# Kernel tuning notes

Hardware: AMD Instinct MI355X
Metric: run time of the kernel (lower is better)

Reference implementation:

```python
import jax, jax.numpy as jnp
import numpy as np

SIZE = 5   # local window side
HEADS = 1

def patch_extract(x, size):
    # x: [B, C, H, W] -> [B, C, size*size, H, W], replicate padding,
    # window index l = i*size + j (row-major over kernel), matching F.unfold.
    p = size // 2
    xp = jnp.pad(x, ((0, 0), (0, 0), (p, p), (p, p)), mode='edge')
    H, W = x.shape[2], x.shape[3]
    windows = [xp[:, :, i:i + H, j:j + W] for i in range(size) for j in range(size)]
    return jnp.stack(windows, axis=2)

def setup_inputs() -> dict:
    key = jax.random.key(0)
    k1, k2, k3, k4 = jax.random.split(key, 4)
    B, C, H, W = 4, 128, 64, 128
    attn = jax.random.normal(k1, (B, HEADS, H * W, SIZE * SIZE), dtype=jnp.float32)
    fmap = jax.random.normal(k2, (B, C, H, W), dtype=jnp.float32)
    Wv = jax.random.normal(k3, (C, C), dtype=jnp.float32) * (1.0 / np.sqrt(C))
    gamma = jax.random.normal(k4, (1,), dtype=jnp.float32)
    return {"attn": attn, "fmap": fmap, "Wv": Wv, "gamma": gamma}

def reference(attn, fmap, Wv, gamma):
    B, C, H, W = fmap.shape
    d = C // HEADS
    L = SIZE * SIZE
    # to_v: 1x1 conv, no bias
    v = jnp.einsum('oc,bchw->bohw', Wv, fmap)
    # local window gather: [B, C, L, H, W]
    v = patch_extract(v, SIZE)
    # 'b (h d) l x y -> b h (x y) d l'
    v = v.reshape(B, HEADS, d, L, H, W)
    v = v.transpose(0, 1, 4, 5, 2, 3).reshape(B, HEADS, H * W, d, L)
    # weighted sum over the local window
    out = jnp.einsum('bhnl,bhndl->bhnd', attn, v)
    # 'b h (x y) d -> b (h d) x y'
    out = out.reshape(B, HEADS, H, W, d).transpose(0, 1, 4, 2, 3).reshape(B, C, H, W)
    return fmap + gamma[0] * out
```

## Files before the change

### kernel.cpp

```cpp
#include <hip/hip_runtime.h>


namespace {
constexpr int Bn = 4, Cn = 128, Hn = 64, Wn = 128, Ln = 25;
constexpr int HWn = Hn * Wn;

constexpr int TY = 4, TX = 16;
constexpr int HY = 8, HX = 24;
constexpr int RS = 136;
constexpr int SVS = 136;
constexpr int WVS = 136;
constexpr int NT = 512;

typedef __attribute__((ext_vector_type(8))) short short8;
typedef __attribute__((ext_vector_type(4))) float f32x4;

__device__ inline unsigned short f2bf(float f) {
    unsigned u = __float_as_uint(f);
    return (unsigned short)((u + 0x7fffu + ((u >> 16) & 1u)) >> 16);
}

__global__ __launch_bounds__(NT, 4) void lsa_fused(
    const float* __restrict__ attn, const float* __restrict__ fmap,
    const float* __restrict__ Wv, const float* __restrict__ gamma,
    float* __restrict__ out)
{
    __shared__ alignas(16) unsigned short hs[HY * HX * RS];
    __shared__ alignas(16) unsigned short sv[TY * TX * SVS];
    __shared__ float at_s[TY * TX * Ln];

    const int tid = threadIdx.x;
    const int b = blockIdx.z;
    const int x0 = blockIdx.x * TX;
    const int y0 = blockIdx.y * TY;

    for (int i = tid; i < HY * 64 * 6; i += NT) {
        const int k = i % 6;
        const int r = i / 6;
        const int cp = r & 63;
        const int dy = r >> 6;
        const int ry = min(max(y0 + dy - 2, 0), Hn - 1);
        const int gxb = x0 - 4 + 4 * k;
        const size_t rowb = ((size_t)(b * Cn + 2 * cp)) * HWn + (size_t)ry * Wn;
        float4 va, vb;
        if (gxb < 0) {
            const float s0 = fmap[rowb], s1 = fmap[rowb + HWn];
            va.x = va.y = va.z = va.w = s0;
            vb.x = vb.y = vb.z = vb.w = s1;
        } else if (gxb > Wn - 4) {
            const float s0 = fmap[rowb + Wn - 1], s1 = fmap[rowb + HWn + Wn - 1];
            va.x = va.y = va.z = va.w = s0;
            vb.x = vb.y = vb.z = vb.w = s1;
        } else {
            va = *(const float4*)&fmap[rowb + gxb];
            vb = *(const float4*)&fmap[rowb + HWn + gxb];
        }
        unsigned short* hbase = &hs[(dy * HX + 4 * k) * RS + 2 * cp];
        *(unsigned*)&hbase[0 * RS] = (unsigned)f2bf(va.x) | ((unsigned)f2bf(vb.x) << 16);
        *(unsigned*)&hbase[1 * RS] = (unsigned)f2bf(va.y) | ((unsigned)f2bf(vb.y) << 16);
        *(unsigned*)&hbase[2 * RS] = (unsigned)f2bf(va.z) | ((unsigned)f2bf(vb.z) << 16);
        *(unsigned*)&hbase[3 * RS] = (unsigned)f2bf(va.w) | ((unsigned)f2bf(vb.w) << 16);
    }
    {
        const size_t ab = ((size_t)b * HWn + (size_t)y0 * Wn + x0) * Ln;
        for (int i = tid; i < TY * TX * Ln; i += NT) {
            const int yi = i / 400, j = i - yi * 400;
            at_s[i] = attn[ab + (size_t)yi * (Wn * Ln) + j];
        }
    }
    __syncthreads();

    const int xi = tid & 15, kq = (tid >> 4) & 7, yi = tid >> 7;
    const int p = yi * 16 + xi;
    float acc[16];
#pragma unroll
    for (int j = 0; j < 16; ++j) acc[j] = 0.f;

#pragma unroll
    for (int l = 0; l < Ln; ++l) {
        const int dy = l / 5, dx = l % 5;
        const float a = at_s[p * Ln + l];
        const unsigned short* row = &hs[((yi + dy) * HX + (2 + xi + dx)) * RS + kq * 16];
#pragma unroll
        for (int q = 0; q < 2; ++q) {
            uint4 u = *(const uint4*)&row[q * 8];
            const unsigned w[4] = {u.x, u.y, u.z, u.w};
#pragma unroll
            for (int e = 0; e < 4; ++e) {
                acc[q * 8 + 2 * e + 0] += a * __uint_as_float(w[e] << 16);
                acc[q * 8 + 2 * e + 1] += a * __uint_as_float(w[e] & 0xffff0000u);
            }
        }
    }
    {
        unsigned short* dst = &sv[p * SVS + kq * 16];
#pragma unroll
        for (int q = 0; q < 2; ++q) {
            unsigned pk[4];
#pragma unroll
            for (int e = 0; e < 4; ++e)
                pk[e] = (unsigned)f2bf(acc[q * 8 + 2 * e]) |
                        ((unsigned)f2bf(acc[q * 8 + 2 * e + 1]) << 16);
            uint4 v; v.x = pk[0]; v.y = pk[1]; v.z = pk[2]; v.w = pk[3];
            *(uint4*)&dst[q * 8] = v;
        }
    }
    __syncthreads();

#pragma unroll
    for (int t = 0; t < 8; ++t) {
        const int i4 = tid + t * NT;
        const float4 w = *(const float4*)&Wv[(size_t)i4 * 4];
        const int r = i4 >> 5;
        const int c = (i4 & 31) * 4;
        uint2 v;
        v.x = (unsigned)f2bf(w.x) | ((unsigned)f2bf(w.y) << 16);
        v.y = (unsigned)f2bf(w.z) | ((unsigned)f2bf(w.w) << 16);
        *(uint2*)&hs[r * WVS + c] = v;
    }
    __syncthreads();

    const int wave = tid >> 6, lane = tid & 63;
    const int m16 = lane & 15, q = lane >> 4;
    const int wrow = wave >> 1;
    const int mhalf = wave & 1;
    const int n = (y0 + wrow) * Wn + x0 + m16;
    const float g = gamma[0];

    short8 bfrag[4];
    {
        const unsigned short* srow = &sv[(wrow * 16 + m16) * SVS + q * 8];
#pragma unroll
        for (int kk = 0; kk < 4; ++kk) bfrag[kk] = *(const short8*)(srow + kk * 32);
    }
    f32x4 accv[4];
#pragma unroll
    for (int t = 0; t < 4; ++t) { f32x4 z = {0.f, 0.f, 0.f, 0.f}; accv[t] = z; }

#pragma unroll
    for (int t = 0; t < 4; ++t) {
        const int mg = mhalf * 4 + t;
        const unsigned short* arow = &hs[(mg * 16 + m16) * WVS + q * 8];
#pragma unroll
        for (int kk = 0; kk < 4; ++kk) {
            short8 af = *(const short8*)(arow + kk * 32);
            accv[t] = __builtin_amdgcn_mfma_f32_16x16x32_bf16(af, bfrag[kk], accv[t], 0, 0, 0);
        }
    }

#pragma unroll
    for (int t = 0; t < 4; ++t) {
        const int mg = mhalf * 4 + t;
#pragma unroll
        for (int r = 0; r < 4; ++r) {
            const int c = mg * 16 + q * 4 + r;
            const size_t idx = ((size_t)(b * Cn + c)) * HWn + n;
            out[idx] = fmap[idx] + g * accv[t][r];
        }
    }
}
}

extern "C" void kernel_launch(void* const* d_in, const int* in_sizes, int n_in,
                              void* d_out, int out_size, void* d_ws, size_t ws_size,
                              hipStream_t stream) {
    const float* attn  = (const float*)d_in[0];
    const float* fmap  = (const float*)d_in[1];
    const float* Wv    = (const float*)d_in[2];
    const float* gamma = (const float*)d_in[3];
    float* out = (float*)d_out;

    dim3 grid(Wn / TX, Hn / TY, Bn);
    lsa_fused<<<grid, NT, 0, stream>>>(attn, fmap, Wv, gamma, out);
}
```

Measured before the change: 98.97 us.

## Batch global loads into registers before LDS stores and swizzle block order

The halo fill now issues all six fmap load pairs and the attn tile load into registers before any conversion or LDS write. The attn load becomes a single float4 per thread. The Wv load is hoisted above the sv pack so its latency overlaps that work. The 3D grid is flattened to 512 blocks and remapped so neighbouring block IDs spread across spatial tiles, intended to balance L2 or XCD locality. The extra live float4 registers raise register pressure under the 4-blocks-per-SIMD launch bound and may cause spills.

Measured after the change: 90.20 us. 8.9% less time.

```diff
diff --git a/kernel.cpp b/kernel.cpp
--- a/kernel.cpp
+++ b/kernel.cpp
@@ -27,14 +27,23 @@
 {
     __shared__ alignas(16) unsigned short hs[HY * HX * RS];
     __shared__ alignas(16) unsigned short sv[TY * TX * SVS];
-    __shared__ float at_s[TY * TX * Ln];
+    __shared__ alignas(16) float at_s[TY * TX * Ln];
 
     const int tid = threadIdx.x;
-    const int b = blockIdx.z;
-    const int x0 = blockIdx.x * TX;
-    const int y0 = blockIdx.y * TY;
 
-    for (int i = tid; i < HY * 64 * 6; i += NT) {
+    const unsigned bid = blockIdx.x;
+    const unsigned logical = (bid & 7u) * 64u + (bid >> 3);
+    const int bx  = logical & 7;
+    const int byz = logical >> 3;
+    const int by  = byz & 15;
+    const int b   = byz >> 4;
+    const int x0 = bx * TX;
+    const int y0 = by * TY;
+
+    float4 va[6], vb[6];
+#pragma unroll
+    for (int t = 0; t < 6; ++t) {
+        const int i = tid + t * NT;
         const int k = i % 6;
         const int r = i / 6;
         const int cp = r & 63;
@@ -42,32 +51,40 @@
         const int ry = min(max(y0 + dy - 2, 0), Hn - 1);
         const int gxb = x0 - 4 + 4 * k;
         const size_t rowb = ((size_t)(b * Cn + 2 * cp)) * HWn + (size_t)ry * Wn;
-        float4 va, vb;
         if (gxb < 0) {
             const float s0 = fmap[rowb], s1 = fmap[rowb + HWn];
-            va.x = va.y = va.z = va.w = s0;
-            vb.x = vb.y = vb.z = vb.w = s1;
+            va[t].x = va[t].y = va[t].z = va[t].w = s0;
+            vb[t].x = vb[t].y = vb[t].z = vb[t].w = s1;
         } else if (gxb > Wn - 4) {
             const float s0 = fmap[rowb + Wn - 1], s1 = fmap[rowb + HWn + Wn - 1];
-            va.x = va.y = va.z = va.w = s0;
-            vb.x = vb.y = vb.z = vb.w = s1;
+            va[t].x = va[t].y = va[t].z = va[t].w = s0;
+            vb[t].x = vb[t].y = vb[t].z = vb[t].w = s1;
         } else {
-            va = *(const float4*)&fmap[rowb + gxb];
-            vb = *(const float4*)&fmap[rowb + HWn + gxb];
-        }
-        unsigned short* hbase = &hs[(dy * HX + 4 * k) * RS + 2 * cp];
-        *(unsigned*)&hbase[0 * RS] = (unsigned)f2bf(va.x) | ((unsigned)f2bf(vb.x) << 16);
-        *(unsigned*)&hbase[1 * RS] = (unsigned)f2bf(va.y) | ((unsigned)f2bf(vb.y) << 16);
-        *(unsigned*)&hbase[2 * RS] = (unsigned)f2bf(va.z) | ((unsigned)f2bf(vb.z) << 16);
-        *(unsigned*)&hbase[3 * RS] = (unsigned)f2bf(va.w) | ((unsigned)f2bf(vb.w) << 16);
-    }
-    {
-        const size_t ab = ((size_t)b * HWn + (size_t)y0 * Wn + x0) * Ln;
-        for (int i = tid; i < TY * TX * Ln; i += NT) {
-            const int yi = i / 400, j = i - yi * 400;
-            at_s[i] = attn[ab + (size_t)yi * (Wn * Ln) + j];
+            va[t] = *(const float4*)&fmap[rowb + gxb];
+            vb[t] = *(const float4*)&fmap[rowb + HWn + gxb];
         }
     }
+    float4 at_r;
+    const int yi_a = tid / 100, j4 = tid - yi_a * 100;
+    if (tid < 400) {
+        const size_t ab = ((size_t)b * HWn + (size_t)y0 * Wn + x0) * Ln;
+        at_r = *(const float4*)&attn[ab + (size_t)yi_a * (Wn * Ln) + j4 * 4];
+    }
+
+#pragma unroll
+    for (int t = 0; t < 6; ++t) {
+        const int i = tid + t * NT;
+        const int k = i % 6;
+        const int r = i / 6;
+        const int cp = r & 63;
+        const int dy = r >> 6;
+        unsigned short* hbase = &hs[(dy * HX + 4 * k) * RS + 2 * cp];
+        *(unsigned*)&hbase[0 * RS] = (unsigned)f2bf(va[t].x) | ((unsigned)f2bf(vb[t].x) << 16);
+        *(unsigned*)&hbase[1 * RS] = (unsigned)f2bf(va[t].y) | ((unsigned)f2bf(vb[t].y) << 16);
+        *(unsigned*)&hbase[2 * RS] = (unsigned)f2bf(va[t].z) | ((unsigned)f2bf(vb[t].z) << 16);
+        *(unsigned*)&hbase[3 * RS] = (unsigned)f2bf(va[t].w) | ((unsigned)f2bf(vb[t].w) << 16);
+    }
+    if (tid < 400) *(float4*)&at_s[tid * 4] = at_r;
     __syncthreads();
 
     const int xi = tid & 15, kq = (tid >> 4) & 7, yi = tid >> 7;
@@ -92,6 +109,11 @@
             }
         }
     }
+    float4 wq[8];
+#pragma unroll
+    for (int t = 0; t < 8; ++t)
+        wq[t] = *(const float4*)&Wv[(size_t)(tid + t * NT) * 4];
+
     {
         unsigned short* dst = &sv[p * SVS + kq * 16];
 #pragma unroll
@@ -110,12 +132,11 @@
 #pragma unroll
     for (int t = 0; t < 8; ++t) {
         const int i4 = tid + t * NT;
-        const float4 w = *(const float4*)&Wv[(size_t)i4 * 4];
         const int r = i4 >> 5;
         const int c = (i4 & 31) * 4;
         uint2 v;
-        v.x = (unsigned)f2bf(w.x) | ((unsigned)f2bf(w.y) << 16);
-        v.y = (unsigned)f2bf(w.z) | ((unsigned)f2bf(w.w) << 16);
+        v.x = (unsigned)f2bf(wq[t].x) | ((unsigned)f2bf(wq[t].y) << 16);
+        v.y = (unsigned)f2bf(wq[t].z) | ((unsigned)f2bf(wq[t].w) << 16);
         *(uint2*)&hs[r * WVS + c] = v;
     }
     __syncthreads();
@@ -170,6 +191,5 @@
     const float* gamma = (const float*)d_in[3];
     float* out = (float*)d_out;
 
-    dim3 grid(Wn / TX, Hn / TY, Bn);
-    lsa_fused<<<grid, NT, 0, stream>>>(attn, fmap, Wv, gamma, out);
+    lsa_fused<<<dim3(512), NT, 0, stream>>>(attn, fmap, Wv, gamma, out);
 }
```
